# Optimization experiments

Measured on AMD Instinct MI355X. Metric: run time of the kernel, lower is better.

## Reference

```python
import jax, jax.numpy as jnp
import numpy as np

S, N, D, H = 1024, 8, 1024, 16
DK = D // H
SCALE = np.sqrt(DK).astype(np.float32)


def setup_inputs() -> dict:
    key = jax.random.key(0)
    ks = jax.random.split(key, 16)
    f32 = jnp.float32
    Qpoi = jax.random.normal(ks[0], (S, N, D), f32)
    Qsvi = jax.random.normal(ks[1], (S, N, D), f32)
    K = jax.random.normal(ks[2], (S, N, D), f32)
    V = jax.random.normal(ks[3], (S, N, D), f32)
    # padding mask: True = masked key; random valid lengths in [S//2, S]
    lengths = jax.random.randint(ks[4], (N,), S // 2, S + 1)
    key_padding_mask = jnp.arange(S)[None, :] >= lengths[:, None]  # [N, S] bool
    w = 0.02
    wq_poi_w = jax.random.normal(ks[5], (D, D), f32) * w
    wq_poi_b = jnp.zeros((D,), f32)
    wq_svi_w = jax.random.normal(ks[6], (D, D), f32) * w
    wq_svi_b = jnp.zeros((D,), f32)
    wk_w = jax.random.normal(ks[7], (D, D), f32) * w
    wk_b = jnp.zeros((D,), f32)
    wv_w = jax.random.normal(ks[8], (D, D), f32) * w
    wv_b = jnp.zeros((D,), f32)
    fc_w = jax.random.normal(ks[9], (D, D), f32) * w
    fc_b = jnp.zeros((D,), f32)
    return dict(Qpoi=Qpoi, Qsvi=Qsvi, K=K, V=V, key_padding_mask=key_padding_mask,
                wq_poi_w=wq_poi_w, wq_poi_b=wq_poi_b, wq_svi_w=wq_svi_w, wq_svi_b=wq_svi_b,
                wk_w=wk_w, wk_b=wk_b, wv_w=wv_w, wv_b=wv_b, fc_w=fc_w, fc_b=fc_b)


def _proj_heads(x, W, b):
    # x: [S, N, D] -> linear -> [N, H, S, DK]
    y = x @ W.T + b                      # [S, N, D]
    y = jnp.transpose(y, (1, 0, 2))      # [N, S, D]
    y = y.reshape(N, S, H, DK)
    return jnp.transpose(y, (0, 2, 1, 3))  # [N, H, S, DK]


def _attend(Qh, Kh, Vh, mask):
    # Qh,Kh,Vh: [N, H, S, DK]; mask: [N, S] bool (True = masked)
    scores = jnp.einsum('nhqd,nhkd->nhqk', Qh, Kh) / SCALE
    scores = jnp.where(mask[:, None, None, :], -jnp.inf, scores)
    attn = jax.nn.softmax(scores, axis=-1)  # dropout is identity in eval
    out = jnp.einsum('nhqk,nhkd->nhqd', attn, Vh)
    out = jnp.transpose(out, (0, 2, 1, 3)).reshape(N, S, D)  # [N, S, D]
    return out


def reference(Qpoi, Qsvi, K, V, key_padding_mask,
              wq_poi_w, wq_poi_b, wq_svi_w, wq_svi_b,
              wk_w, wk_b, wv_w, wv_b, fc_w, fc_b):
    Qp = _proj_heads(Qpoi, wq_poi_w, wq_poi_b)
    Qs = _proj_heads(Qsvi, wq_svi_w, wq_svi_b)
    Kh = _proj_heads(K, wk_w, wk_b)
    Vh = _proj_heads(V, wv_w, wv_b)
    poi = _attend(Qp, Kh, Vh, key_padding_mask)
    svi = _attend(Qs, Kh, Vh, key_padding_mask)
    poi_out = jnp.transpose(poi @ fc_w.T + fc_b, (1, 0, 2))  # [S, N, D]
    svi_out = jnp.transpose(svi @ fc_w.T + fc_b, (1, 0, 2))
    return (poi_out, svi_out)
```

## Files before the change

kernel.cpp:

```cpp
#include <hip/hip_runtime.h>

typedef unsigned short u16;
typedef unsigned int u32;
typedef short bf16x8 __attribute__((ext_vector_type(8)));
typedef float f32x4 __attribute__((ext_vector_type(4)));

__device__ __forceinline__ u16 f2bf(float f) {
  union { float f; u32 i; } v; v.f = f;
  u32 x = v.i;
  return (u16)((x + 0x7fffu + ((x >> 16) & 1u)) >> 16);
}

union Pack16 { u16 h[16]; float4 f4[2]; };

__device__ __forceinline__ void gld16(const u16* g, u16* l) {
  __builtin_amdgcn_global_load_lds((const __attribute__((address_space(1))) u32*)g,
                                   (__attribute__((address_space(3))) u32*)l, 16, 0, 0);
}

struct C2 { const float* s[2]; u16* d[2]; };
__global__ __launch_bounds__(256) void conv2_kernel(C2 c) {
  const int z = blockIdx.z;
  const size_t i = (size_t)blockIdx.x * 256 + threadIdx.x;
  const float4* s = (const float4*)c.s[z] + i * 2;
  float4 a = s[0], b = s[1];
  union { u16 h[8]; float4 f; } o;
  o.h[0] = f2bf(a.x); o.h[1] = f2bf(a.y); o.h[2] = f2bf(a.z); o.h[3] = f2bf(a.w);
  o.h[4] = f2bf(b.x); o.h[5] = f2bf(b.y); o.h[6] = f2bf(b.z); o.h[7] = f2bf(b.w);
  *(float4*)(c.d[z] + i * 8) = o.f;
}

struct W5 { const float* p[5]; };
__global__ __launch_bounds__(256) void conv_w_kernel(W5 w, u16* __restrict__ dst) {
  const int m = blockIdx.x >> 9;
  const size_t i = (size_t)(blockIdx.x & 511) * 256 + threadIdx.x;
  const float4* s = (const float4*)w.p[m] + i * 2;
  float4 a = s[0], b = s[1];
  union { u16 h[8]; float4 f; } o;
  o.h[0] = f2bf(a.x); o.h[1] = f2bf(a.y); o.h[2] = f2bf(a.z); o.h[3] = f2bf(a.w);
  o.h[4] = f2bf(b.x); o.h[5] = f2bf(b.y); o.h[6] = f2bf(b.z); o.h[7] = f2bf(b.w);
  *(float4*)(dst + ((size_t)m << 20) + i * 8) = o.f;
}

template<int ASRC>
__device__ __forceinline__ const u16* aAddr(const u16* A, int row, int k) {
  if constexpr (ASRC == 0) {
    return A + (size_t)row * 1024 + k;
  } else {
    const int n = row >> 10, s = row & 1023, h = k >> 6;
    return A + ((size_t)((n * 16 + h) * 1024 + s)) * 64 + (k & 63);
  }
}

struct GB { const void* A[2]; const void* W[2]; const float* bias[2]; void* out[2]; };

template<int MODEA, int MODEB, int ASRC, int WBF>
__global__ __launch_bounds__(256, 2) void gemm_bt(GB gb) {
  __shared__ __align__(16) u16 At[128 * 32];
  __shared__ __align__(16) u16 Bt[128 * 32];

  const int z = blockIdx.z;
  const u16* Ab = (const u16*)gb.A[z];
  const u16* Wb = (const u16*)gb.W[z];
  const float* bias = gb.bias[z];
  void* outv = gb.out[z];
  const int mode = z ? MODEB : MODEA;

  const int tid = threadIdx.x;
  const int lane = tid & 63, wave = tid >> 6;
  const int quad = lane >> 4, l16 = lane & 15;
  const int bm = blockIdx.y * 128, bn = blockIdx.x * 128;
  const int wm = (wave >> 1) * 64, wn = (wave & 1) * 64;

  const int r0 = wave * 32;
  const int lrow = lane >> 2;
  const int lk = (lane & 3) * 8;

  const int srow = tid >> 1, scol = (tid & 1) * 16;

  f32x4 acc[4][4];
#pragma unroll
  for (int i = 0; i < 4; i++)
#pragma unroll
    for (int j = 0; j < 4; j++) acc[i][j] = (f32x4){0.f, 0.f, 0.f, 0.f};

  for (int k0 = 0; k0 < 1024; k0 += 32) {
    float4 wf[4];
    if constexpr (!WBF) {
      const float* wp = (const float*)Wb + (size_t)(bn + srow) * 1024 + k0 + scol;
#pragma unroll
      for (int q = 0; q < 4; q++) wf[q] = ((const float4*)wp)[q];
    }
    __syncthreads();
    gld16(aAddr<ASRC>(Ab, bm + r0 + lrow, k0 + lk), At + r0 * 32);
    gld16(aAddr<ASRC>(Ab, bm + r0 + 16 + lrow, k0 + lk), At + (r0 + 16) * 32);
    if constexpr (WBF) {
      gld16(Wb + (size_t)(bn + r0 + lrow) * 1024 + k0 + lk, Bt + r0 * 32);
      gld16(Wb + (size_t)(bn + r0 + 16 + lrow) * 1024 + k0 + lk, Bt + (r0 + 16) * 32);
    } else {
      Pack16 pb;
#pragma unroll
      for (int q = 0; q < 4; q++) {
        pb.h[q * 4 + 0] = f2bf(wf[q].x);
        pb.h[q * 4 + 1] = f2bf(wf[q].y);
        pb.h[q * 4 + 2] = f2bf(wf[q].z);
        pb.h[q * 4 + 3] = f2bf(wf[q].w);
      }
      *(float4*)(Bt + srow * 32 + scol) = pb.f4[0];
      *(float4*)(Bt + srow * 32 + scol + 8) = pb.f4[1];
    }
    __syncthreads();

    bf16x8 af[4], bfr[4];
#pragma unroll
    for (int mt = 0; mt < 4; mt++)
      af[mt] = *(const bf16x8*)(At + (wm + mt * 16 + l16) * 32 + quad * 8);
#pragma unroll
    for (int nt = 0; nt < 4; nt++)
      bfr[nt] = *(const bf16x8*)(Bt + (wn + nt * 16 + l16) * 32 + quad * 8);
#pragma unroll
    for (int mt = 0; mt < 4; mt++)
#pragma unroll
      for (int nt = 0; nt < 4; nt++)
        acc[mt][nt] = __builtin_amdgcn_mfma_f32_16x16x32_bf16(af[mt], bfr[nt], acc[mt][nt], 0, 0, 0);
  }

#pragma unroll
  for (int mt = 0; mt < 4; mt++) {
#pragma unroll
    for (int nt = 0; nt < 4; nt++) {
      const int col = bn + wn + nt * 16 + l16;
      const float bv = bias[col];
#pragma unroll
      for (int i = 0; i < 4; i++) {
        const int row = bm + wm + mt * 16 + quad * 4 + i;
        const float v = acc[mt][nt][i] + bv;
        if (mode == 0) {
          const int s = row >> 3, n = row & 7;
          const int h = col >> 6, dk = col & 63;
          ((u16*)outv)[(size_t)(((n * 16 + h) * 1024 + s) * 64 + dk)] = f2bf(v);
        } else if (mode == 1) {
          const int n = row >> 10, s = row & 1023;
          ((float*)outv)[(size_t)((s * 8 + n) * 1024 + col)] = v;
        } else {
          const int s = row >> 3, n = row & 7;
          const int h = col >> 6, dk = col & 63;
          ((u16*)outv)[(size_t)(((n * 16 + h) * 64 + dk) * 1024 + s)] = f2bf(v);
        }
      }
    }
  }
}

__global__ __launch_bounds__(256, 2) void attn2_kernel(const u16* __restrict__ Qs_g,
                                                       const u16* __restrict__ Qp_g,
                                                       const u16* __restrict__ K,
                                                       const u16* __restrict__ Vt_g,
                                                       const int* __restrict__ mask,
                                                       u16* __restrict__ OUTs,
                                                       u16* __restrict__ OUTp) {
  __shared__ __align__(16) u16 Ks[64 * 72];
  __shared__ __align__(16) u16 Vt[64 * 64];
  __shared__ __align__(16) u16 PsS[4 * 16 * 72];
  __shared__ __align__(16) u16 PsP[4 * 16 * 72];
  __shared__ float mbias[64];

  const int tid = threadIdx.x;
  const int lane = tid & 63, wave = tid >> 6;
  const int quad = lane >> 4, l16 = lane & 15;
  const int qt = blockIdx.x, nh = blockIdx.y;
  const int n = nh >> 4;
  const size_t base = (size_t)nh << 16;

  const int q0 = qt * 64 + wave * 16;
  bf16x8 qS0, qS1, qP0, qP1;
  {
    const u16* qp = Qs_g + base + (size_t)(q0 + l16) * 64 + quad * 8;
    qS0 = *(const bf16x8*)qp;
    qS1 = *(const bf16x8*)(qp + 32);
    const u16* qq = Qp_g + base + (size_t)(q0 + l16) * 64 + quad * 8;
    qP0 = *(const bf16x8*)qq;
    qP1 = *(const bf16x8*)(qq + 32);
  }

  float mS[4], mP[4];
  f32x4 oS[4], oP[4], lS, lP;
#pragma unroll
  for (int i = 0; i < 4; i++) { mS[i] = -1e30f; mP[i] = -1e30f; }
#pragma unroll
  for (int d = 0; d < 4; d++) { oS[d] = (f32x4){0.f, 0.f, 0.f, 0.f}; oP[d] = (f32x4){0.f, 0.f, 0.f, 0.f}; }
  lS = (f32x4){0.f, 0.f, 0.f, 0.f};
  lP = (f32x4){0.f, 0.f, 0.f, 0.f};

  bf16x8 vbOnes;
  {
    const short ob = (l16 == 0) ? (short)0x3F80 : (short)0;
#pragma unroll
    for (int j = 0; j < 8; j++) vbOnes[j] = ob;
  }

  const int sr = tid >> 2;
  const int sc = (tid & 3) * 16;
  const u16* kbase = K + base + (size_t)sr * 64 + sc;
  const u16* vbase = Vt_g + base + (size_t)sr * 1024 + sc;
  u16* vdst0 = Vt + sr * 64 + ((((sc >> 3) + 0) ^ (sr & 7)) << 3);
  u16* vdst1 = Vt + sr * 64 + ((((sc >> 3) + 1) ^ (sr & 7)) << 3);
  u16* pwS = PsS + wave * (16 * 72);
  u16* pwP = PsP + wave * (16 * 72);

  for (int kt = 0; kt < 16; kt++) {
    float4 kv0 = *(const float4*)(kbase + kt * 64 * 64);
    float4 kv1 = *(const float4*)(kbase + kt * 64 * 64 + 8);
    float4 vv0 = *(const float4*)(vbase + kt * 64);
    float4 vv1 = *(const float4*)(vbase + kt * 64 + 8);
    int mk = (tid < 64) ? mask[n * 1024 + kt * 64 + tid] : 0;
    __syncthreads();
    *(float4*)(Ks + sr * 72 + sc) = kv0;
    *(float4*)(Ks + sr * 72 + sc + 8) = kv1;
    *(float4*)vdst0 = vv0;
    *(float4*)vdst1 = vv1;
    if (tid < 64) mbias[tid] = mk ? -1e30f : 0.0f;
    __syncthreads();

    f32x4 sS[4], sP[4];
#pragma unroll
    for (int nt = 0; nt < 4; nt++) {
      bf16x8 b0 = *(const bf16x8*)(Ks + (nt * 16 + l16) * 72 + quad * 8);
      bf16x8 b1 = *(const bf16x8*)(Ks + (nt * 16 + l16) * 72 + 32 + quad * 8);
      f32x4 a = (f32x4){0.f, 0.f, 0.f, 0.f};
      a = __builtin_amdgcn_mfma_f32_16x16x32_bf16(qS0, b0, a, 0, 0, 0);
      a = __builtin_amdgcn_mfma_f32_16x16x32_bf16(qS1, b1, a, 0, 0, 0);
      sS[nt] = a;
      f32x4 c = (f32x4){0.f, 0.f, 0.f, 0.f};
      c = __builtin_amdgcn_mfma_f32_16x16x32_bf16(qP0, b0, c, 0, 0, 0);
      c = __builtin_amdgcn_mfma_f32_16x16x32_bf16(qP1, b1, c, 0, 0, 0);
      sP[nt] = c;
    }
    float mb[4];
#pragma unroll
    for (int nt = 0; nt < 4; nt++) mb[nt] = mbias[nt * 16 + l16];
#pragma unroll
    for (int nt = 0; nt < 4; nt++)
#pragma unroll
      for (int i = 0; i < 4; i++) {
        sS[nt][i] = sS[nt][i] * 0.125f + mb[nt];
        sP[nt][i] = sP[nt][i] * 0.125f + mb[nt];
      }

#pragma unroll
    for (int i = 0; i < 4; i++) {
      float m = fmaxf(fmaxf(sS[0][i], sS[1][i]), fmaxf(sS[2][i], sS[3][i]));
#pragma unroll
      for (int off = 1; off < 16; off <<= 1) m = fmaxf(m, __shfl_xor(m, off, 64));
      float mn = fmaxf(mS[i], m);
      float alpha = __expf(mS[i] - mn);
      mS[i] = mn;
#pragma unroll
      for (int d = 0; d < 4; d++) oS[d][i] *= alpha;
      lS[i] *= alpha;
    }
#pragma unroll
    for (int i = 0; i < 4; i++) {
      float m = fmaxf(fmaxf(sP[0][i], sP[1][i]), fmaxf(sP[2][i], sP[3][i]));
#pragma unroll
      for (int off = 1; off < 16; off <<= 1) m = fmaxf(m, __shfl_xor(m, off, 64));
      float mn = fmaxf(mP[i], m);
      float alpha = __expf(mP[i] - mn);
      mP[i] = mn;
#pragma unroll
      for (int d = 0; d < 4; d++) oP[d][i] *= alpha;
      lP[i] *= alpha;
    }
#pragma unroll
    for (int nt = 0; nt < 4; nt++)
#pragma unroll
      for (int i = 0; i < 4; i++) {
        pwS[(quad * 4 + i) * 72 + nt * 16 + l16] = f2bf(__expf(sS[nt][i] - mS[i]));
        pwP[(quad * 4 + i) * 72 + nt * 16 + l16] = f2bf(__expf(sP[nt][i] - mP[i]));
      }
    __syncthreads();

#pragma unroll
    for (int ks = 0; ks < 2; ks++) {
      bf16x8 paS = *(const bf16x8*)(pwS + l16 * 72 + ks * 32 + quad * 8);
      bf16x8 paP = *(const bf16x8*)(pwP + l16 * 72 + ks * 32 + quad * 8);
      lS = __builtin_amdgcn_mfma_f32_16x16x32_bf16(paS, vbOnes, lS, 0, 0, 0);
      lP = __builtin_amdgcn_mfma_f32_16x16x32_bf16(paP, vbOnes, lP, 0, 0, 0);
#pragma unroll
      for (int d = 0; d < 4; d++) {
        bf16x8 vb = *(const bf16x8*)(Vt + (d * 16 + l16) * 64 +
                                     (((ks * 4 + quad) ^ (l16 & 7)) << 3));
        oS[d] = __builtin_amdgcn_mfma_f32_16x16x32_bf16(paS, vb, oS[d], 0, 0, 0);
        oP[d] = __builtin_amdgcn_mfma_f32_16x16x32_bf16(paP, vb, oP[d], 0, 0, 0);
      }
    }
  }

#pragma unroll
  for (int i = 0; i < 4; i++) {
    const float lsv = __shfl(lS[i], lane & 48, 64);
    const float lpv = __shfl(lP[i], lane & 48, 64);
    const float invS = 1.0f / lsv;
    const float invP = 1.0f / lpv;
    const int q = q0 + quad * 4 + i;
    const size_t ob = base + (size_t)q * 64;
#pragma unroll
    for (int d = 0; d < 4; d++) {
      OUTs[ob + d * 16 + l16] = f2bf(oS[d][i] * invS);
      OUTp[ob + d * 16 + l16] = f2bf(oP[d][i] * invP);
    }
  }
}

extern "C" void kernel_launch(void* const* d_in, const int* in_sizes, int n_in,
                              void* d_out, int out_size, void* d_ws, size_t ws_size,
                              hipStream_t stream) {
  const float* Qpoi = (const float*)d_in[0];
  const float* Qsvi = (const float*)d_in[1];
  const float* Kin  = (const float*)d_in[2];
  const float* Vin  = (const float*)d_in[3];
  const int* mask   = (const int*)d_in[4];
  const float* wq_poi_w = (const float*)d_in[5];
  const float* wq_poi_b = (const float*)d_in[6];
  const float* wq_svi_w = (const float*)d_in[7];
  const float* wq_svi_b = (const float*)d_in[8];
  const float* wk_w = (const float*)d_in[9];
  const float* wk_b = (const float*)d_in[10];
  const float* wv_w = (const float*)d_in[11];
  const float* wv_b = (const float*)d_in[12];
  const float* fc_w = (const float*)d_in[13];
  const float* fc_b = (const float*)d_in[14];

  const size_t SZ = (size_t)8 * 16 * 1024 * 64;
  const size_t WBE = (size_t)5 << 20;
  u16* W0 = (u16*)d_ws;
  u16* W1 = W0 + SZ;
  u16* Wp = W1 + SZ;
  const bool haveWb = ws_size >= (2 * SZ + WBE) * sizeof(u16);

  float* Of = (float*)d_out;
  u16* R0 = (u16*)d_out;
  u16* R1 = R0 + SZ;
  u16* R2 = R0 + 2 * SZ;
  u16* R3 = R0 + 3 * SZ;

  dim3 bb(256, 1, 1);
  dim3 gg(8, 64, 2);
  dim3 ga(16, 128);
  dim3 gc(4096, 1, 2);

  if (haveWb) {
    W5 w5{{wk_w, wv_w, wq_svi_w, wq_poi_w, fc_w}};
    hipLaunchKernelGGL(conv_w_kernel, dim3(2560), bb, 0, stream, w5, Wp);
  }
  const u16* Wk  = Wp + ((size_t)0 << 20);
  const u16* Wv  = Wp + ((size_t)1 << 20);
  const u16* Wqs = Wp + ((size_t)2 << 20);
  const u16* Wqp = Wp + ((size_t)3 << 20);
  const u16* Wfc = Wp + ((size_t)4 << 20);

  {
    C2 c{{Kin, Vin}, {R0, R1}};
    hipLaunchKernelGGL(conv2_kernel, gc, bb, 0, stream, c);
    GB g{{R0, R1},
         {haveWb ? (const void*)Wk : (const void*)wk_w, haveWb ? (const void*)Wv : (const void*)wv_w},
         {wk_b, wv_b}, {(void*)W0, (void*)W1}};
    if (haveWb) hipLaunchKernelGGL((gemm_bt<0, 2, 0, 1>), gg, bb, 0, stream, g);
    else        hipLaunchKernelGGL((gemm_bt<0, 2, 0, 0>), gg, bb, 0, stream, g);
  }

  {
    C2 c{{Qsvi, Qpoi}, {R0, R1}};
    hipLaunchKernelGGL(conv2_kernel, gc, bb, 0, stream, c);
    GB g{{R0, R1},
         {haveWb ? (const void*)Wqs : (const void*)wq_svi_w, haveWb ? (const void*)Wqp : (const void*)wq_poi_w},
         {wq_svi_b, wq_poi_b}, {(void*)R2, (void*)R3}};
    if (haveWb) hipLaunchKernelGGL((gemm_bt<0, 0, 0, 1>), gg, bb, 0, stream, g);
    else        hipLaunchKernelGGL((gemm_bt<0, 0, 0, 0>), gg, bb, 0, stream, g);
  }

  hipLaunchKernelGGL(attn2_kernel, ga, bb, 0, stream,
                     (const u16*)R2, (const u16*)R3, (const u16*)W0, (const u16*)W1,
                     mask, R2, R3);

  hipMemcpyAsync(W0, R3, SZ * sizeof(u16), hipMemcpyDeviceToDevice, stream);
  hipMemcpyAsync(W1, R2, SZ * sizeof(u16), hipMemcpyDeviceToDevice, stream);
  {
    GB g{{W0, W1},
         {haveWb ? (const void*)Wfc : (const void*)fc_w, haveWb ? (const void*)Wfc : (const void*)fc_w},
         {fc_b, fc_b}, {(void*)Of, (void*)(Of + SZ)}};
    if (haveWb) hipLaunchKernelGGL((gemm_bt<1, 1, 1, 1>), gg, bb, 0, stream, g);
    else        hipLaunchKernelGGL((gemm_bt<1, 1, 1, 0>), gg, bb, 0, stream, g);
  }
}
```

Measured before the change: 534.6 us.

## Double-buffer GEMM LDS tiles and prefetch next K/V tile in attention

The GEMM kernel now uses two LDS buffers for the A and W tiles and issues loads for the next k-step before computing on the current one. This removes one barrier per iteration and overlaps global-to-LDS transfers with MFMA work. The fp32 weight register loads are pipelined two steps ahead. In the attention kernel, K, V and mask loads for the next key tile are issued right after the LDS stores so their latency overlaps the score and softmax math. The cost is doubled GEMM LDS use, which may affect the 2-blocks-per-CU occupancy, plus extra live registers.

New measurement: 572.2 us. 1.07x slower.

```diff
diff --git a/kernel.cpp b/kernel.cpp
--- a/kernel.cpp
+++ b/kernel.cpp
@@ -56,8 +56,8 @@
 
 template<int MODEA, int MODEB, int ASRC, int WBF>
 __global__ __launch_bounds__(256, 2) void gemm_bt(GB gb) {
-  __shared__ __align__(16) u16 At[128 * 32];
-  __shared__ __align__(16) u16 Bt[128 * 32];
+  __shared__ __align__(16) u16 At[2][128 * 32];
+  __shared__ __align__(16) u16 Bt[2][128 * 32];
 
   const int z = blockIdx.z;
   const u16* Ab = (const u16*)gb.A[z];
@@ -75,6 +75,7 @@
   const int r0 = wave * 32;
   const int lrow = lane >> 2;
   const int lk = (lane & 3) * 8;
+  (void)lrow;
 
   const int srow = tid >> 1, scol = (tid & 1) * 16;
 
@@ -84,19 +85,23 @@
 #pragma unroll
     for (int j = 0; j < 4; j++) acc[i][j] = (f32x4){0.f, 0.f, 0.f, 0.f};
 
-  for (int k0 = 0; k0 < 1024; k0 += 32) {
-    float4 wf[4];
-    if constexpr (!WBF) {
-      const float* wp = (const float*)Wb + (size_t)(bn + srow) * 1024 + k0 + scol;
-#pragma unroll
-      for (int q = 0; q < 4; q++) wf[q] = ((const float4*)wp)[q];
-    }
-    __syncthreads();
-    gld16(aAddr<ASRC>(Ab, bm + r0 + lrow, k0 + lk), At + r0 * 32);
-    gld16(aAddr<ASRC>(Ab, bm + r0 + 16 + lrow, k0 + lk), At + (r0 + 16) * 32);
+  float4 wf[4];
+
+  auto loadWf = [&](int k0) {
+    const float* wp = (const float*)Wb + (size_t)(bn + srow) * 1024 + k0 + scol;
+#pragma unroll
+    for (int q = 0; q < 4; q++) wf[q] = ((const float4*)wp)[q];
+  };
+  auto stageA = [&](int b, int k0) {
+    const int row = bm + r0 + (lane >> 2);
+    gld16(aAddr<ASRC>(Ab, row, k0 + lk), At[b] + r0 * 32);
+    gld16(aAddr<ASRC>(Ab, row + 16, k0 + lk), At[b] + (r0 + 16) * 32);
+  };
+  auto stageW = [&](int b, int k0) {
     if constexpr (WBF) {
-      gld16(Wb + (size_t)(bn + r0 + lrow) * 1024 + k0 + lk, Bt + r0 * 32);
-      gld16(Wb + (size_t)(bn + r0 + 16 + lrow) * 1024 + k0 + lk, Bt + (r0 + 16) * 32);
+      const int row = bn + r0 + (lane >> 2);
+      gld16(Wb + (size_t)row * 1024 + k0 + lk, Bt[b] + r0 * 32);
+      gld16(Wb + (size_t)(row + 16) * 1024 + k0 + lk, Bt[b] + (r0 + 16) * 32);
     } else {
       Pack16 pb;
 #pragma unroll
@@ -106,18 +111,32 @@
         pb.h[q * 4 + 2] = f2bf(wf[q].z);
         pb.h[q * 4 + 3] = f2bf(wf[q].w);
       }
-      *(float4*)(Bt + srow * 32 + scol) = pb.f4[0];
-      *(float4*)(Bt + srow * 32 + scol + 8) = pb.f4[1];
-    }
+      *(float4*)(Bt[b] + srow * 32 + scol) = pb.f4[0];
+      *(float4*)(Bt[b] + srow * 32 + scol + 8) = pb.f4[1];
+    }
+  };
+
+  if constexpr (!WBF) loadWf(0);
+  stageA(0, 0);
+  stageW(0, 0);
+  if constexpr (!WBF) loadWf(32);
+
+  for (int t = 0; t < 32; ++t) {
+    const int cb = t & 1, nb = cb ^ 1;
     __syncthreads();
+    if (t + 1 < 32) {
+      stageA(nb, (t + 1) * 32);
+      stageW(nb, (t + 1) * 32);
+      if constexpr (!WBF) if (t + 2 < 32) loadWf((t + 2) * 32);
+    }
 
     bf16x8 af[4], bfr[4];
 #pragma unroll
     for (int mt = 0; mt < 4; mt++)
-      af[mt] = *(const bf16x8*)(At + (wm + mt * 16 + l16) * 32 + quad * 8);
+      af[mt] = *(const bf16x8*)(At[cb] + (wm + mt * 16 + l16) * 32 + quad * 8);
 #pragma unroll
     for (int nt = 0; nt < 4; nt++)
-      bfr[nt] = *(const bf16x8*)(Bt + (wn + nt * 16 + l16) * 32 + quad * 8);
+      bfr[nt] = *(const bf16x8*)(Bt[cb] + (wn + nt * 16 + l16) * 32 + quad * 8);
 #pragma unroll
     for (int mt = 0; mt < 4; mt++)
 #pragma unroll
@@ -208,12 +227,13 @@
   u16* pwS = PsS + wave * (16 * 72);
   u16* pwP = PsP + wave * (16 * 72);
 
+  float4 kv0 = *(const float4*)(kbase);
+  float4 kv1 = *(const float4*)(kbase + 8);
+  float4 vv0 = *(const float4*)(vbase);
+  float4 vv1 = *(const float4*)(vbase + 8);
+  int mk = (tid < 64) ? mask[n * 1024 + tid] : 0;
+
   for (int kt = 0; kt < 16; kt++) {
-    float4 kv0 = *(const float4*)(kbase + kt * 64 * 64);
-    float4 kv1 = *(const float4*)(kbase + kt * 64 * 64 + 8);
-    float4 vv0 = *(const float4*)(vbase + kt * 64);
-    float4 vv1 = *(const float4*)(vbase + kt * 64 + 8);
-    int mk = (tid < 64) ? mask[n * 1024 + kt * 64 + tid] : 0;
     __syncthreads();
     *(float4*)(Ks + sr * 72 + sc) = kv0;
     *(float4*)(Ks + sr * 72 + sc + 8) = kv1;
@@ -221,6 +241,14 @@
     *(float4*)vdst1 = vv1;
     if (tid < 64) mbias[tid] = mk ? -1e30f : 0.0f;
     __syncthreads();
+
+    if (kt + 1 < 16) {
+      kv0 = *(const float4*)(kbase + (kt + 1) * 64 * 64);
+      kv1 = *(const float4*)(kbase + (kt + 1) * 64 * 64 + 8);
+      vv0 = *(const float4*)(vbase + (kt + 1) * 64);
+      vv1 = *(const float4*)(vbase + (kt + 1) * 64 + 8);
+      mk = (tid < 64) ? mask[n * 1024 + (kt + 1) * 64 + tid] : 0;
+    }
 
     f32x4 sS[4], sP[4];
 #pragma unroll
```
